# Kernel tuning notes

Measured on AMD Instinct MI355X. Metric: run time of the kernel, lower is better.

Reference implementation:

```python
import jax, jax.numpy as jnp
import numpy as np

N_HEADS = 16
N_EMBD = 1024
HEAD_DIM = N_EMBD // N_HEADS
WINDOW = 512
B, T = 2, 2048


def setup_inputs() -> dict:
    key = jax.random.key(0)
    ks = jax.random.split(key, 5)
    s = 0.02
    return {
        "x": jax.random.normal(ks[0], (B, T, N_EMBD), dtype=jnp.float32),
        "Wq": jax.random.normal(ks[1], (N_EMBD, N_EMBD), dtype=jnp.float32) * s,
        "Wk": jax.random.normal(ks[2], (N_EMBD, N_EMBD), dtype=jnp.float32) * s,
        "Wv": jax.random.normal(ks[3], (N_EMBD, N_EMBD), dtype=jnp.float32) * s,
        "Wo": jax.random.normal(ks[4], (N_EMBD, N_EMBD), dtype=jnp.float32) * s,
    }


def _sliding_window_mask(T, window):
    # mask[i, j] True iff max(0, i-window+1) <= j <= i  (causal banded)
    i = jnp.arange(T)[:, None]
    j = jnp.arange(T)[None, :]
    return (j <= i) & (j > i - window)


def reference(x, Wq, Wk, Wv, Wo):
    Bb, Tt, C = x.shape
    # nn.Linear applies x @ W.T; we store W as [in, out] so just x @ W
    def heads(w):
        return (x @ w).reshape(Bb, Tt, N_HEADS, HEAD_DIM).transpose(0, 2, 1, 3)
    q, k, v = heads(Wq), heads(Wk), heads(Wv)  # [B, H, T, D]
    scores = jnp.einsum("bhqd,bhkd->bhqk", q, k) / jnp.sqrt(jnp.float32(HEAD_DIM))
    mask = _sliding_window_mask(Tt, WINDOW)  # [T, T]
    scores = jnp.where(mask[None, None], scores, jnp.float32(-jnp.inf))
    attn = jax.nn.softmax(scores, axis=-1)
    out = jnp.einsum("bhqk,bhkd->bhqd", attn, v)  # [B, H, T, D]
    out = out.transpose(0, 2, 1, 3).reshape(Bb, Tt, C)
    return out @ Wo
```

## Files before the change

kernel.cpp:

```cpp
#include <hip/hip_runtime.h>

#define B_SZ 2
#define T_SZ 2048
#define C_SZ 1024
#define K_SZ 1024
#define QKV_LD 3072
#define H_CNT 16
#define D_SZ 64
#define WIN 512

typedef __bf16 bf16_t;
typedef bf16_t bf16x8 __attribute__((ext_vector_type(8)));
typedef bf16_t bf16x4 __attribute__((ext_vector_type(4)));
typedef float f32x4 __attribute__((ext_vector_type(4)));
typedef unsigned int u32;

__device__ __forceinline__ f32x4 mfma16(bf16x8 a, bf16x8 b, f32x4 c) {
  return __builtin_amdgcn_mfma_f32_16x16x32_bf16(a, b, c, 0, 0, 0);
}

__device__ __forceinline__ void gload_lds16(const void* gsrc, void* ldst) {
  auto g = (__attribute__((address_space(1))) void*)(unsigned long long)gsrc;
  auto l = (__attribute__((address_space(3))) void*)(unsigned int)(unsigned long long)ldst;
  __builtin_amdgcn_global_load_lds(g, l, 16, 0, 0);
}

__global__ __launch_bounds__(256) void prep(
    const float* __restrict__ x, bf16_t* __restrict__ xb,
    const float* __restrict__ W0, const float* __restrict__ W1,
    const float* __restrict__ W2, const float* __restrict__ W3,
    bf16_t* __restrict__ T0, bf16_t* __restrict__ T1,
    bf16_t* __restrict__ T2, bf16_t* __restrict__ T3) {
  if (blockIdx.z == 4) {
    const int base = (blockIdx.y * 32 + blockIdx.x) * 256 + threadIdx.x;
#pragma unroll
    for (int j = 0; j < 4; ++j) {
      const int idx = base + j * 262144;
      const float4 v = ((const float4*)x)[idx];
      bf16x4 r;
      r[0] = (bf16_t)v.x; r[1] = (bf16_t)v.y; r[2] = (bf16_t)v.z; r[3] = (bf16_t)v.w;
      ((bf16x4*)xb)[idx] = r;
    }
    return;
  }
  __shared__ float tile[32][33];
  const float* W = blockIdx.z == 0 ? W0 : blockIdx.z == 1 ? W1 : blockIdx.z == 2 ? W2 : W3;
  bf16_t* Tt = blockIdx.z == 0 ? T0 : blockIdx.z == 1 ? T1 : blockIdx.z == 2 ? T2 : T3;
  const int tx = threadIdx.x & 31, ty = threadIdx.x >> 5;
  const int r0 = blockIdx.y * 32, c0 = blockIdx.x * 32;
#pragma unroll
  for (int i = 0; i < 4; ++i)
    tile[ty + i * 8][tx] = W[(size_t)(r0 + ty + i * 8) * C_SZ + c0 + tx];
  __syncthreads();
#pragma unroll
  for (int i = 0; i < 4; ++i)
    Tt[(size_t)(c0 + ty + i * 8) * C_SZ + r0 + tx] = (bf16_t)tile[tx][ty + i * 8];
}

__global__ __launch_bounds__(256) void transpose_v(const bf16_t* __restrict__ QKV,
                                                   bf16_t* __restrict__ Vt) {
  __shared__ bf16_t tile[32][33];
  const int t0 = blockIdx.x * 32, d0 = blockIdx.y * 32, bh = blockIdx.z;
  const int b = bh >> 4, h = bh & 15;
  const int tx = threadIdx.x & 31, ty = threadIdx.x >> 5;
#pragma unroll
  for (int i = 0; i < 4; ++i)
    tile[ty + i * 8][tx] =
        QKV[((size_t)b * T_SZ + t0 + ty + i * 8) * QKV_LD + 2048 + h * D_SZ + d0 + tx];
  __syncthreads();
#pragma unroll
  for (int i = 0; i < 4; ++i)
    Vt[((size_t)bh * D_SZ + d0 + ty + i * 8) * T_SZ + t0 + tx] = tile[tx][ty + i * 8];
}

#define GM_NT 16

__global__ __launch_bounds__(512, 2) void gemm256(
    const bf16_t* __restrict__ A, const bf16_t* __restrict__ Bt,
    bf16_t* __restrict__ C) {
  __shared__ __align__(16) bf16_t As[2][256 * 64];
  __shared__ __align__(16) bf16_t Bs[2][192 * 64];
  const int wg = blockIdx.x + 16 * blockIdx.y;
  const int swz = (wg & 7) * 32 + (wg >> 3);
  const int bx = swz & 15, by = swz >> 4;
  const int m0 = by * 256, n0 = bx * 192;
  const int tid = threadIdx.x, w = tid >> 6, lane = tid & 63;
  const int wr = w >> 2, wc = w & 3;
  const int g = lane >> 4, l15 = lane & 15, sw = l15 & 7;
  const int srow = lane >> 3, sj = lane & 7;

  f32x4 acc[8][3] = {};

  auto stageA = [&](int buf, int half, int k0) {
#pragma unroll
    for (int q8 = 0; q8 < 2; ++q8) {
      const int rg = w * 16 + q8 * 8;
      gload_lds16(A + (size_t)(m0 + half * 128 + rg + srow) * K_SZ + k0 + ((sj ^ srow) << 3),
                  &As[buf][half * 8192 + rg * 64]);
    }
  };
  auto stageB = [&](int buf, int third, int k0) {
    const int rg = third * 64 + w * 8;
    gload_lds16(Bt + (size_t)(n0 + rg + srow) * K_SZ + k0 + ((sj ^ srow) << 3),
                &Bs[buf][rg * 64]);
  };

  stageA(0, 0, 0); stageA(0, 1, 0);
  stageB(0, 0, 0); stageB(0, 1, 0); stageB(0, 2, 0);

#define LDAF(MF4, MH, KK) \
  (*(const bf16x8*)&As[buf][(wr * 128 + ((MH) * 4 + (MF4)) * 16 + l15) * 64 + \
                            ((((KK) << 2) | g) ^ sw) * 8])
#define LDBF(NF, KK) \
  (*(const bf16x8*)&Bs[buf][(wc * 48 + (NF) * 16 + l15) * 64 + \
                            ((((KK) << 2) | g) ^ sw) * 8])
#define MROW(MH, MF, AF)                                   \
  acc[(MH) * 4 + (MF)][0] = mfma16(AF, bf0, acc[(MH) * 4 + (MF)][0]); \
  acc[(MH) * 4 + (MF)][1] = mfma16(AF, bf1, acc[(MH) * 4 + (MF)][1]); \
  acc[(MH) * 4 + (MF)][2] = mfma16(AF, bf2, acc[(MH) * 4 + (MF)][2]);

#pragma unroll 2
  for (int t = 0; t < GM_NT; ++t) {
    const int buf = t & 1, nb = buf ^ 1;
    const int k1 = (t + 1) * 64;
    asm volatile("s_waitcnt vmcnt(0)" ::: "memory");
    __builtin_amdgcn_s_barrier();

    bf16x8 bf0, bf1, bf2;
    {
      bf16x8 a0 = LDAF(0, 0, 0), a1 = LDAF(1, 0, 0), a2 = LDAF(2, 0, 0), a3 = LDAF(3, 0, 0);
      bf0 = LDBF(0, 0); bf1 = LDBF(1, 0); bf2 = LDBF(2, 0);
      if (t < GM_NT - 1) { stageA(nb, 0, k1); stageA(nb, 1, k1); }
      __builtin_amdgcn_s_barrier();
      __builtin_amdgcn_s_setprio(1);
      MROW(0, 0, a0) MROW(0, 1, a1) MROW(0, 2, a2) MROW(0, 3, a3)
      __builtin_amdgcn_s_setprio(0);
      __builtin_amdgcn_s_barrier();
    }
    {
      bf16x8 a0 = LDAF(0, 1, 0), a1 = LDAF(1, 1, 0), a2 = LDAF(2, 1, 0), a3 = LDAF(3, 1, 0);
      if (t < GM_NT - 1) { stageB(nb, 0, k1); stageB(nb, 1, k1); stageB(nb, 2, k1); }
      __builtin_amdgcn_s_barrier();
      __builtin_amdgcn_s_setprio(1);
      MROW(1, 0, a0) MROW(1, 1, a1) MROW(1, 2, a2) MROW(1, 3, a3)
      __builtin_amdgcn_s_setprio(0);
      __builtin_amdgcn_s_barrier();
    }
    {
      bf16x8 a0 = LDAF(0, 0, 1), a1 = LDAF(1, 0, 1), a2 = LDAF(2, 0, 1), a3 = LDAF(3, 0, 1);
      bf0 = LDBF(0, 1); bf1 = LDBF(1, 1); bf2 = LDBF(2, 1);
      __builtin_amdgcn_s_barrier();
      __builtin_amdgcn_s_setprio(1);
      MROW(0, 0, a0) MROW(0, 1, a1) MROW(0, 2, a2) MROW(0, 3, a3)
      __builtin_amdgcn_s_setprio(0);
      __builtin_amdgcn_s_barrier();
    }
    {
      bf16x8 a0 = LDAF(0, 1, 1), a1 = LDAF(1, 1, 1), a2 = LDAF(2, 1, 1), a3 = LDAF(3, 1, 1);
      __builtin_amdgcn_s_barrier();
      __builtin_amdgcn_s_setprio(1);
      MROW(1, 0, a0) MROW(1, 1, a1) MROW(1, 2, a2) MROW(1, 3, a3)
      __builtin_amdgcn_s_setprio(0);
    }
  }

#pragma unroll
  for (int mf = 0; mf < 8; ++mf)
#pragma unroll
    for (int nf = 0; nf < 3; ++nf)
#pragma unroll
      for (int i = 0; i < 4; ++i)
        C[(size_t)(m0 + wr * 128 + mf * 16 + g * 4 + i) * QKV_LD +
          n0 + wc * 48 + nf * 16 + l15] = (bf16_t)acc[mf][nf][i];
}

__global__ __launch_bounds__(512, 4) void gemm128(
    const bf16_t* __restrict__ A, int lda, const bf16_t* __restrict__ Bt,
    float* __restrict__ C, int N) {
  __shared__ __align__(16) bf16_t As[2][128 * 64];
  __shared__ __align__(16) bf16_t Bs[2][128 * 64];
  const int wg = blockIdx.x + 8 * blockIdx.y;
  const int swz = (wg & 7) * 32 + (wg >> 3);
  const int bx = swz & 7, by = swz >> 3;
  const int m0 = by * 128, n0 = bx * 128;
  const int tid = threadIdx.x, w = tid >> 6, lane = tid & 63;
  const int wr = w >> 2, wc = w & 3;
  const int g = lane >> 4, l15 = lane & 15, sw = l15 & 7;
  const int srow = lane >> 3, sj = lane & 7;

  f32x4 acc[4][2] = {};

  auto stage = [&](int buf, int k0) {
#pragma unroll
    for (int half = 0; half < 2; ++half) {
      const int rg = half * 64 + w * 8;
      gload_lds16(A + (size_t)(m0 + rg + srow) * lda + k0 + ((sj ^ srow) << 3),
                  &As[buf][rg * 64]);
      gload_lds16(Bt + (size_t)(n0 + rg + srow) * K_SZ + k0 + ((sj ^ srow) << 3),
                  &Bs[buf][rg * 64]);
    }
  };

  stage(0, 0);

#pragma unroll 2
  for (int t = 0; t < GM_NT; ++t) {
    const int buf = t & 1;
    asm volatile("s_waitcnt vmcnt(0)" ::: "memory");
    __builtin_amdgcn_s_barrier();
    if (t < GM_NT - 1) stage(buf ^ 1, (t + 1) * 64);
#pragma unroll
    for (int kk = 0; kk < 2; ++kk) {
      bf16x8 af[4], bfr[2];
#pragma unroll
      for (int mf = 0; mf < 4; ++mf)
        af[mf] = *(const bf16x8*)&As[buf][(wr * 64 + mf * 16 + l15) * 64 +
                                          (((kk << 2) | g) ^ sw) * 8];
#pragma unroll
      for (int nf = 0; nf < 2; ++nf)
        bfr[nf] = *(const bf16x8*)&Bs[buf][(wc * 32 + nf * 16 + l15) * 64 +
                                           (((kk << 2) | g) ^ sw) * 8];
      __builtin_amdgcn_s_setprio(1);
#pragma unroll
      for (int mf = 0; mf < 4; ++mf)
#pragma unroll
        for (int nf = 0; nf < 2; ++nf)
          acc[mf][nf] = mfma16(af[mf], bfr[nf], acc[mf][nf]);
      __builtin_amdgcn_s_setprio(0);
    }
  }

#pragma unroll
  for (int mf = 0; mf < 4; ++mf)
#pragma unroll
    for (int nf = 0; nf < 2; ++nf)
#pragma unroll
      for (int i = 0; i < 4; ++i)
        C[(size_t)(m0 + wr * 64 + mf * 16 + g * 4 + i) * N +
          n0 + wc * 32 + nf * 16 + l15] = acc[mf][nf][i];
}

__global__ __launch_bounds__(256) void attn_kernel(
    bf16_t* __restrict__ QKV, const bf16_t* __restrict__ Vt) {
  __shared__ __align__(16) bf16_t Kl[2][64 * 64];
  __shared__ __align__(16) bf16_t Vl[2][64 * 64];

  const int qt = ((blockIdx.x & 7) << 2) | (blockIdx.x >> 3);
  const int bh = blockIdx.y;
  const int b = bh >> 4, h = bh & 15;
  const int q0 = qt * 64;
  const int tid = threadIdx.x, w = tid >> 6, lane = tid & 63;
  const int g = lane >> 4, l15 = lane & 15, gh = g >> 1;
  const int wrow0 = q0 + w * 16;
  const int myrow = wrow0 + l15;
  const int sub = lane >> 3, jj = lane & 7;
  const int sw = l15 & 7;

  auto stage = [&](int bufi, int kt) {
#pragma unroll
    for (int cc = 0; cc < 2; ++cc) {
      const int chunk = w * 2 + cc;
      const int row = chunk * 8 + sub;
      const int sj = jj ^ sub;
      gload_lds16(QKV + ((size_t)b * T_SZ + kt + row) * QKV_LD + 1024 + h * D_SZ + sj * 8,
                  &Kl[bufi][chunk * 512]);
      gload_lds16(Vt + ((size_t)bh * D_SZ + row) * T_SZ + kt + sj * 8,
                  &Vl[bufi][chunk * 512]);
    }
  };

  bf16x8 qf[2];
  {
    const bf16_t* qptr = QKV + ((size_t)b * T_SZ + myrow) * QKV_LD + h * D_SZ;
    const float QSC = 0.125f * 1.44269504f;
#pragma unroll
    for (int c2 = 0; c2 < 2; ++c2) {
      bf16x8 t = *(const bf16x8*)(qptr + c2 * 32 + g * 8);
      bf16x8 o;
#pragma unroll
      for (int j = 0; j < 8; ++j) o[j] = (bf16_t)((float)t[j] * QSC);
      qf[c2] = o;
    }
  }

  float m_s = -1e30f, l_s = 0.f;
  f32x4 oacc[4] = {};

  int kstart = q0 - (WIN - 1);
  if (kstart < 0) kstart = 0;
  kstart &= ~63;
  const int nt = (q0 + 64 - kstart) >> 6;

  stage(0, kstart);

  for (int it = 0; it < nt; ++it) {
    const int kt = kstart + (it << 6);
    const int cur = it & 1;
    if (it + 1 < nt) {
      stage(cur ^ 1, kt + 64);
      asm volatile("s_waitcnt vmcnt(4)" ::: "memory");
    } else {
      asm volatile("s_waitcnt vmcnt(0)" ::: "memory");
    }
    __builtin_amdgcn_s_barrier();
    __builtin_amdgcn_sched_barrier(0);

    f32x4 s[4] = {};
#pragma unroll
    for (int t = 0; t < 4; ++t) {
      const bf16_t* kbase = &Kl[cur][(t * 16 + l15) * 64];
#pragma unroll
      for (int c2 = 0; c2 < 2; ++c2) {
        const bf16x8 kf = *(const bf16x8*)(kbase + (((c2 * 4 + g) ^ sw) << 3));
        s[t] = mfma16(kf, qf[c2], s[t]);
      }
    }

    const bool interior = (kt + 63 <= wrow0) && (kt >= wrow0 + 15 - (WIN - 1));
    float sv[4][4];
    if (interior) {
#pragma unroll
      for (int t = 0; t < 4; ++t)
#pragma unroll
        for (int i = 0; i < 4; ++i) sv[t][i] = s[t][i];
    } else {
#pragma unroll
      for (int t = 0; t < 4; ++t)
#pragma unroll
        for (int i = 0; i < 4; ++i) {
          const int kk = kt + t * 16 + g * 4 + i;
          sv[t][i] = (kk <= myrow && kk > myrow - WIN) ? s[t][i] : -1e30f;
        }
    }

    float mx = sv[0][0];
#pragma unroll
    for (int t = 0; t < 4; ++t)
#pragma unroll
      for (int i = 0; i < 4; ++i)
        if (t || i) mx = fmaxf(mx, sv[t][i]);
    mx = fmaxf(mx, __shfl_xor(mx, 16));
    mx = fmaxf(mx, __shfl_xor(mx, 32));

    float mbase;
    const bool defer = __all(mx <= m_s + 8.f);
    if (defer) {
      mbase = m_s;
    } else {
      const float mnew = fmaxf(m_s, mx);
      const float scl = exp2f(m_s - mnew);
      m_s = mnew;
      mbase = (mnew > -1e29f) ? mnew : 1e30f;
      float sc4[4];
#pragma unroll
      for (int i = 0; i < 4; ++i) sc4[i] = __shfl(scl, g * 4 + i, 16);
#pragma unroll
      for (int c = 0; c < 4; ++c)
#pragma unroll
        for (int i = 0; i < 4; ++i) oacc[c][i] *= sc4[i];
      l_s *= scl;
    }

    float p[4][4];
    float rsum = 0.f;
#pragma unroll
    for (int t = 0; t < 4; ++t)
#pragma unroll
      for (int i = 0; i < 4; ++i) {
        p[t][i] = exp2f(sv[t][i] - mbase);
        rsum += p[t][i];
      }
    rsum += __shfl_xor(rsum, 16);
    rsum += __shfl_xor(rsum, 32);
    l_s += rsum;

    u32 Wp[4][2];
#pragma unroll
    for (int t = 0; t < 4; ++t)
#pragma unroll
      for (int w2 = 0; w2 < 2; ++w2) {
        union { bf16_t hh[2]; u32 uu; } pk;
        pk.hh[0] = (bf16_t)p[t][2 * w2];
        pk.hh[1] = (bf16_t)p[t][2 * w2 + 1];
        Wp[t][w2] = pk.uu;
      }

#pragma unroll
    for (int kp = 0; kp < 2; ++kp) {
      const u32 lo0 = Wp[2 * kp][0], lo1 = Wp[2 * kp][1];
      const u32 hi0 = Wp[2 * kp + 1][0], hi1 = Wp[2 * kp + 1][1];
      union { u32 u[4]; bf16x8 v; } pa;
      pa.u[0] = gh ? hi0 : lo0;
      pa.u[1] = gh ? hi1 : lo1;
      pa.u[2] = (u32)__shfl_xor((int)(gh ? lo0 : hi0), 32);
      pa.u[3] = (u32)__shfl_xor((int)(gh ? lo1 : hi1), 32);

      const int tA = 2 * kp + gh;
      const int low = (g & 1) * 4;
      const int cA = ((tA * 2 + gh) ^ sw) << 3;
      const int cB = ((tA * 2 + (gh ^ 1)) ^ sw) << 3;
#pragma unroll
      for (int c = 0; c < 4; ++c) {
        const bf16_t* vbase = &Vl[cur][(c * 16 + l15) * 64];
        union { bf16x4 h[2]; bf16x8 v; } vv;
        vv.h[0] = *(const bf16x4*)(vbase + cA + low);
        vv.h[1] = *(const bf16x4*)(vbase + cB + low);
        oacc[c] = mfma16(pa.v, vv.v, oacc[c]);
      }
    }
    __builtin_amdgcn_sched_barrier(0);
    __builtin_amdgcn_s_barrier();
  }

  const float invl = 1.0f / l_s;
  float inv4[4];
#pragma unroll
  for (int i = 0; i < 4; ++i) inv4[i] = __shfl(invl, g * 4 + i, 16);
#pragma unroll
  for (int i = 0; i < 4; ++i) {
    const size_t ro = ((size_t)b * T_SZ + wrow0 + g * 4 + i) * QKV_LD + 2048 + h * D_SZ;
#pragma unroll
    for (int c = 0; c < 4; ++c)
      QKV[ro + c * 16 + l15] = (bf16_t)(oacc[c][i] * inv4[i]);
  }
}

extern "C" void kernel_launch(void* const* d_in, const int* in_sizes, int n_in,
                              void* d_out, int out_size, void* d_ws, size_t ws_size,
                              hipStream_t stream) {
  const float* x = (const float*)d_in[0];
  const float* Wq = (const float*)d_in[1];
  const float* Wk = (const float*)d_in[2];
  const float* Wv = (const float*)d_in[3];
  const float* Wo = (const float*)d_in[4];
  float* out = (float*)d_out;
  char* ws = (char*)d_ws;
  const size_t MB = 1ull << 20;
  bf16_t* xb = (bf16_t*)(ws);
  bf16_t* Vtp = (bf16_t*)(ws);
  bf16_t* QKVb = (bf16_t*)(ws + 8 * MB);
  bf16_t* WqT = (bf16_t*)(ws + 32 * MB);
  bf16_t* WkT = (bf16_t*)(ws + 34 * MB);
  bf16_t* WvT = (bf16_t*)(ws + 36 * MB);
  bf16_t* WoT = (bf16_t*)(ws + 38 * MB);

  prep<<<dim3(32, 32, 5), 256, 0, stream>>>(x, xb, Wq, Wk, Wv, Wo,
                                            WqT, WkT, WvT, WoT);
  gemm256<<<dim3(16, 16), 512, 0, stream>>>(xb, WqT, QKVb);
  transpose_v<<<dim3(64, 2, 32), 256, 0, stream>>>(QKVb, Vtp);
  attn_kernel<<<dim3(T_SZ / 64, B_SZ * H_CNT), 256, 0, stream>>>(QKVb, Vtp);
  gemm128<<<dim3(8, 32), 512, 0, stream>>>(QKVb + 2048, QKV_LD, WoT, out, C_SZ);
}
```

Before: 91.59 us.

## Fuse V transpose into QKV GEMM epilogue and enlarge attention query tiles

The QKV GEMM epilogue now writes the V columns directly in transposed [b,h,d,t] layout, which removes the separate transpose_v kernel launch and its extra global round trip. The attention kernel moves to 128-query tiles with 8 waves per block, so each staged K/V tile is shared across twice as many query rows. Waves whose 16-row slice falls entirely outside the current key tile's band now skip the compute. In exchange, V stores from the GEMM are scattered 8-byte writes, there are half as many attention blocks, and some waves idle on edge tiles.

```diff
diff --git a/kernel.cpp b/kernel.cpp
--- a/kernel.cpp
+++ b/kernel.cpp
@@ -57,27 +57,11 @@
     Tt[(size_t)(c0 + ty + i * 8) * C_SZ + r0 + tx] = (bf16_t)tile[tx][ty + i * 8];
 }
 
-__global__ __launch_bounds__(256) void transpose_v(const bf16_t* __restrict__ QKV,
-                                                   bf16_t* __restrict__ Vt) {
-  __shared__ bf16_t tile[32][33];
-  const int t0 = blockIdx.x * 32, d0 = blockIdx.y * 32, bh = blockIdx.z;
-  const int b = bh >> 4, h = bh & 15;
-  const int tx = threadIdx.x & 31, ty = threadIdx.x >> 5;
-#pragma unroll
-  for (int i = 0; i < 4; ++i)
-    tile[ty + i * 8][tx] =
-        QKV[((size_t)b * T_SZ + t0 + ty + i * 8) * QKV_LD + 2048 + h * D_SZ + d0 + tx];
-  __syncthreads();
-#pragma unroll
-  for (int i = 0; i < 4; ++i)
-    Vt[((size_t)bh * D_SZ + d0 + ty + i * 8) * T_SZ + t0 + tx] = tile[tx][ty + i * 8];
-}
-
 #define GM_NT 16
 
 __global__ __launch_bounds__(512, 2) void gemm256(
     const bf16_t* __restrict__ A, const bf16_t* __restrict__ Bt,
-    bf16_t* __restrict__ C) {
+    bf16_t* __restrict__ C, bf16_t* __restrict__ Vt) {
   __shared__ __align__(16) bf16_t As[2][256 * 64];
   __shared__ __align__(16) bf16_t Bs[2][192 * 64];
   const int wg = blockIdx.x + 16 * blockIdx.y;
@@ -165,13 +149,27 @@
   }
 
 #pragma unroll
-  for (int mf = 0; mf < 8; ++mf)
-#pragma unroll
-    for (int nf = 0; nf < 3; ++nf)
-#pragma unroll
-      for (int i = 0; i < 4; ++i)
-        C[(size_t)(m0 + wr * 128 + mf * 16 + g * 4 + i) * QKV_LD +
-          n0 + wc * 48 + nf * 16 + l15] = (bf16_t)acc[mf][nf][i];
+  for (int mf = 0; mf < 8; ++mf) {
+    const int row = m0 + wr * 128 + mf * 16 + g * 4;
+#pragma unroll
+    for (int nf = 0; nf < 3; ++nf) {
+      const int colb = n0 + wc * 48 + nf * 16;
+      if (colb >= 2048) {
+        const int d = colb - 2048 + l15;
+        const size_t vo =
+            ((size_t)((row >> 11) * 16 + (d >> 6)) * 64 + (d & 63)) * (size_t)T_SZ +
+            (row & (T_SZ - 1));
+        union { bf16_t h4[4]; uint2 u; } pk;
+#pragma unroll
+        for (int i = 0; i < 4; ++i) pk.h4[i] = (bf16_t)acc[mf][nf][i];
+        *(uint2*)(Vt + vo) = pk.u;
+      } else {
+#pragma unroll
+        for (int i = 0; i < 4; ++i)
+          C[(size_t)(row + i) * QKV_LD + colb + l15] = (bf16_t)acc[mf][nf][i];
+      }
+    }
+  }
 }
 
 __global__ __launch_bounds__(512, 4) void gemm128(
@@ -240,15 +238,15 @@
           n0 + wc * 32 + nf * 16 + l15] = acc[mf][nf][i];
 }
 
-__global__ __launch_bounds__(256) void attn_kernel(
+__global__ __launch_bounds__(512) void attn_kernel(
     bf16_t* __restrict__ QKV, const bf16_t* __restrict__ Vt) {
   __shared__ __align__(16) bf16_t Kl[2][64 * 64];
   __shared__ __align__(16) bf16_t Vl[2][64 * 64];
 
-  const int qt = ((blockIdx.x & 7) << 2) | (blockIdx.x >> 3);
+  const int qt = ((blockIdx.x & 7) << 1) | (blockIdx.x >> 3);
   const int bh = blockIdx.y;
   const int b = bh >> 4, h = bh & 15;
-  const int q0 = qt * 64;
+  const int q0 = qt * 128;
   const int tid = threadIdx.x, w = tid >> 6, lane = tid & 63;
   const int g = lane >> 4, l15 = lane & 15, gh = g >> 1;
   const int wrow0 = q0 + w * 16;
@@ -257,16 +255,12 @@
   const int sw = l15 & 7;
 
   auto stage = [&](int bufi, int kt) {
-#pragma unroll
-    for (int cc = 0; cc < 2; ++cc) {
-      const int chunk = w * 2 + cc;
-      const int row = chunk * 8 + sub;
-      const int sj = jj ^ sub;
-      gload_lds16(QKV + ((size_t)b * T_SZ + kt + row) * QKV_LD + 1024 + h * D_SZ + sj * 8,
-                  &Kl[bufi][chunk * 512]);
-      gload_lds16(Vt + ((size_t)bh * D_SZ + row) * T_SZ + kt + sj * 8,
-                  &Vl[bufi][chunk * 512]);
-    }
+    const int row = w * 8 + sub;
+    const int sj = jj ^ sub;
+    gload_lds16(QKV + ((size_t)b * T_SZ + kt + row) * QKV_LD + 1024 + h * D_SZ + sj * 8,
+                &Kl[bufi][w * 512]);
+    gload_lds16(Vt + ((size_t)bh * D_SZ + row) * T_SZ + kt + sj * 8,
+                &Vl[bufi][w * 512]);
   };
 
   bf16x8 qf[2];
@@ -289,7 +283,7 @@
   int kstart = q0 - (WIN - 1);
   if (kstart < 0) kstart = 0;
   kstart &= ~63;
-  const int nt = (q0 + 64 - kstart) >> 6;
+  const int nt = (q0 + 128 - kstart) >> 6;
 
   stage(0, kstart);
 
@@ -298,114 +292,117 @@
     const int cur = it & 1;
     if (it + 1 < nt) {
       stage(cur ^ 1, kt + 64);
-      asm volatile("s_waitcnt vmcnt(4)" ::: "memory");
+      asm volatile("s_waitcnt vmcnt(2)" ::: "memory");
     } else {
       asm volatile("s_waitcnt vmcnt(0)" ::: "memory");
     }
     __builtin_amdgcn_s_barrier();
     __builtin_amdgcn_sched_barrier(0);
 
-    f32x4 s[4] = {};
-#pragma unroll
-    for (int t = 0; t < 4; ++t) {
-      const bf16_t* kbase = &Kl[cur][(t * 16 + l15) * 64];
-#pragma unroll
-      for (int c2 = 0; c2 < 2; ++c2) {
-        const bf16x8 kf = *(const bf16x8*)(kbase + (((c2 * 4 + g) ^ sw) << 3));
-        s[t] = mfma16(kf, qf[c2], s[t]);
+    const bool skip = (kt + 63 < wrow0 - (WIN - 1)) || (kt > wrow0 + 15);
+    if (!skip) {
+      f32x4 s[4] = {};
+#pragma unroll
+      for (int t = 0; t < 4; ++t) {
+        const bf16_t* kbase = &Kl[cur][(t * 16 + l15) * 64];
+#pragma unroll
+        for (int c2 = 0; c2 < 2; ++c2) {
+          const bf16x8 kf = *(const bf16x8*)(kbase + (((c2 * 4 + g) ^ sw) << 3));
+          s[t] = mfma16(kf, qf[c2], s[t]);
+        }
       }
-    }
-
-    const bool interior = (kt + 63 <= wrow0) && (kt >= wrow0 + 15 - (WIN - 1));
-    float sv[4][4];
-    if (interior) {
+
+      const bool interior = (kt + 63 <= wrow0) && (kt >= wrow0 + 15 - (WIN - 1));
+      float sv[4][4];
+      if (interior) {
+#pragma unroll
+        for (int t = 0; t < 4; ++t)
+#pragma unroll
+          for (int i = 0; i < 4; ++i) sv[t][i] = s[t][i];
+      } else {
+#pragma unroll
+        for (int t = 0; t < 4; ++t)
+#pragma unroll
+          for (int i = 0; i < 4; ++i) {
+            const int kk = kt + t * 16 + g * 4 + i;
+            sv[t][i] = (kk <= myrow && kk > myrow - WIN) ? s[t][i] : -1e30f;
+          }
+      }
+
+      float mx = sv[0][0];
 #pragma unroll
       for (int t = 0; t < 4; ++t)
 #pragma unroll
-        for (int i = 0; i < 4; ++i) sv[t][i] = s[t][i];
-    } else {
+        for (int i = 0; i < 4; ++i)
+          if (t || i) mx = fmaxf(mx, sv[t][i]);
+      mx = fmaxf(mx, __shfl_xor(mx, 16));
+      mx = fmaxf(mx, __shfl_xor(mx, 32));
+
+      float mbase;
+      const bool defer = __all((mx <= m_s + 8.f) && (m_s > -1e29f));
+      if (defer) {
+        mbase = m_s;
+      } else {
+        const float mnew = fmaxf(m_s, mx);
+        const float scl = exp2f(m_s - mnew);
+        m_s = mnew;
+        mbase = (mnew > -1e29f) ? mnew : 1e30f;
+        float sc4[4];
+#pragma unroll
+        for (int i = 0; i < 4; ++i) sc4[i] = __shfl(scl, g * 4 + i, 16);
+#pragma unroll
+        for (int c = 0; c < 4; ++c)
+#pragma unroll
+          for (int i = 0; i < 4; ++i) oacc[c][i] *= sc4[i];
+        l_s *= scl;
+      }
+
+      float p[4][4];
+      float rsum = 0.f;
 #pragma unroll
       for (int t = 0; t < 4; ++t)
 #pragma unroll
         for (int i = 0; i < 4; ++i) {
-          const int kk = kt + t * 16 + g * 4 + i;
-          sv[t][i] = (kk <= myrow && kk > myrow - WIN) ? s[t][i] : -1e30f;
+          p[t][i] = exp2f(sv[t][i] - mbase);
+          rsum += p[t][i];
         }
-    }
-
-    float mx = sv[0][0];
-#pragma unroll
-    for (int t = 0; t < 4; ++t)
-#pragma unroll
-      for (int i = 0; i < 4; ++i)
-        if (t || i) mx = fmaxf(mx, sv[t][i]);
-    mx = fmaxf(mx, __shfl_xor(mx, 16));
-    mx = fmaxf(mx, __shfl_xor(mx, 32));
-
-    float mbase;
-    const bool defer = __all(mx <= m_s + 8.f);
-    if (defer) {
-      mbase = m_s;
-    } else {
-      const float mnew = fmaxf(m_s, mx);
-      const float scl = exp2f(m_s - mnew);
-      m_s = mnew;
-      mbase = (mnew > -1e29f) ? mnew : 1e30f;
-      float sc4[4];
-#pragma unroll
-      for (int i = 0; i < 4; ++i) sc4[i] = __shfl(scl, g * 4 + i, 16);
-#pragma unroll
-      for (int c = 0; c < 4; ++c)
-#pragma unroll
-        for (int i = 0; i < 4; ++i) oacc[c][i] *= sc4[i];
-      l_s *= scl;
-    }
-
-    float p[4][4];
-    float rsum = 0.f;
-#pragma unroll
-    for (int t = 0; t < 4; ++t)
-#pragma unroll
-      for (int i = 0; i < 4; ++i) {
-        p[t][i] = exp2f(sv[t][i] - mbase);
-        rsum += p[t][i];
-      }
-    rsum += __shfl_xor(rsum, 16);
-    rsum += __shfl_xor(rsum, 32);
-    l_s += rsum;
-
-    u32 Wp[4][2];
-#pragma unroll
-    for (int t = 0; t < 4; ++t)
-#pragma unroll
-      for (int w2 = 0; w2 < 2; ++w2) {
-        union { bf16_t hh[2]; u32 uu; } pk;
-        pk.hh[0] = (bf16_t)p[t][2 * w2];
-        pk.hh[1] = (bf16_t)p[t][2 * w2 + 1];
-        Wp[t][w2] = pk.uu;
-      }
-
-#pragma unroll
-    for (int kp = 0; kp < 2; ++kp) {
-      const u32 lo0 = Wp[2 * kp][0], lo1 = Wp[2 * kp][1];
-      const u32 hi0 = Wp[2 * kp + 1][0], hi1 = Wp[2 * kp + 1][1];
-      union { u32 u[4]; bf16x8 v; } pa;
-      pa.u[0] = gh ? hi0 : lo0;
-      pa.u[1] = gh ? hi1 : lo1;
-      pa.u[2] = (u32)__shfl_xor((int)(gh ? lo0 : hi0), 32);
-      pa.u[3] = (u32)__shfl_xor((int)(gh ? lo1 : hi1), 32);
-
-      const int tA = 2 * kp + gh;
-      const int low = (g & 1) * 4;
-      const int cA = ((tA * 2 + gh) ^ sw) << 3;
-      const int cB = ((tA * 2 + (gh ^ 1)) ^ sw) << 3;
-#pragma unroll
-      for (int c = 0; c < 4; ++c) {
-        const bf16_t* vbase = &Vl[cur][(c * 16 + l15) * 64];
-        union { bf16x4 h[2]; bf16x8 v; } vv;
-        vv.h[0] = *(const bf16x4*)(vbase + cA + low);
-        vv.h[1] = *(const bf16x4*)(vbase + cB + low);
-        oacc[c] = mfma16(pa.v, vv.v, oacc[c]);
+      rsum += __shfl_xor(rsum, 16);
+      rsum += __shfl_xor(rsum, 32);
+      l_s += rsum;
+
+      u32 Wp[4][2];
+#pragma unroll
+      for (int t = 0; t < 4; ++t)
+#pragma unroll
+        for (int w2 = 0; w2 < 2; ++w2) {
+          union { bf16_t hh[2]; u32 uu; } pk;
+          pk.hh[0] = (bf16_t)p[t][2 * w2];
+          pk.hh[1] = (bf16_t)p[t][2 * w2 + 1];
+          Wp[t][w2] = pk.uu;
+        }
+
+#pragma unroll
+      for (int kp = 0; kp < 2; ++kp) {
+        const u32 lo0 = Wp[2 * kp][0], lo1 = Wp[2 * kp][1];
+        const u32 hi0 = Wp[2 * kp + 1][0], hi1 = Wp[2 * kp + 1][1];
+        union { u32 u[4]; bf16x8 v; } pa;
+        pa.u[0] = gh ? hi0 : lo0;
+        pa.u[1] = gh ? hi1 : lo1;
+        pa.u[2] = (u32)__shfl_xor((int)(gh ? lo0 : hi0), 32);
+        pa.u[3] = (u32)__shfl_xor((int)(gh ? lo1 : hi1), 32);
+
+        const int tA = 2 * kp + gh;
+        const int low = (g & 1) * 4;
+        const int cA = ((tA * 2 + gh) ^ sw) << 3;
+        const int cB = ((tA * 2 + (gh ^ 1)) ^ sw) << 3;
+#pragma unroll
+        for (int c = 0; c < 4; ++c) {
+          const bf16_t* vbase = &Vl[cur][(c * 16 + l15) * 64];
+          union { bf16x4 h[2]; bf16x8 v; } vv;
+          vv.h[0] = *(const bf16x4*)(vbase + cA + low);
+          vv.h[1] = *(const bf16x4*)(vbase + cB + low);
+          oacc[c] = mfma16(pa.v, vv.v, oacc[c]);
+        }
       }
     }
     __builtin_amdgcn_sched_barrier(0);
@@ -437,17 +434,16 @@
   char* ws = (char*)d_ws;
   const size_t MB = 1ull << 20;
   bf16_t* xb = (bf16_t*)(ws);
-  bf16_t* Vtp = (bf16_t*)(ws);
   bf16_t* QKVb = (bf16_t*)(ws + 8 * MB);
   bf16_t* WqT = (bf16_t*)(ws + 32 * MB);
   bf16_t* WkT = (bf16_t*)(ws + 34 * MB);
   bf16_t* WvT = (bf16_t*)(ws + 36 * MB);
   bf16_t* WoT = (bf16_t*)(ws + 38 * MB);
+  bf16_t* Vtp = (bf16_t*)(ws + 48 * MB);
 
   prep<<<dim3(32, 32, 5), 256, 0, stream>>>(x, xb, Wq, Wk, Wv, Wo,
                                             WqT, WkT, WvT, WoT);
-  gemm256<<<dim3(16, 16), 512, 0, stream>>>(xb, WqT, QKVb);
-  transpose_v<<<dim3(64, 2, 32), 256, 0, stream>>>(QKVb, Vtp);
-  attn_kernel<<<dim3(T_SZ / 64, B_SZ * H_CNT), 256, 0, stream>>>(QKVb, Vtp);
+  gemm256<<<dim3(16, 16), 512, 0, stream>>>(xb, WqT, QKVb, Vtp);
+  attn_kernel<<<dim3(16, B_SZ * H_CNT), 512, 0, stream>>>(QKVb, Vtp);
   gemm128<<<dim3(8, 32), 512, 0, stream>>>(QKVb + 2048, QKV_LD, WoT, out, C_SZ);
 }
```

New measurement: 86.20 us. 5.9% less time.
